# Kernel tuning notes

Measured on AMD Instinct MI355X. Metric: run time of the kernel, lower is better.

Reference implementation:

```python
import jax, jax.numpy as jnp
import numpy as np

B, N, D, H = 2, 2048, 1024, 16
HD = D // H
SCALE = HD ** -0.5


def setup_inputs() -> dict:
    key = jax.random.key(0)
    ks = jax.random.split(key, 5)
    s = D ** -0.5  # keep activations well-scaled like torch Linear init
    return {
        "x": jax.random.normal(ks[0], (B, N, D), jnp.float32),
        "Wq": jax.random.normal(ks[1], (D, D), jnp.float32) * s,
        "bq": jnp.zeros((D,), jnp.float32),
        "Wk": jax.random.normal(ks[2], (D, D), jnp.float32) * s,
        "bk": jnp.zeros((D,), jnp.float32),
        "Wv": jax.random.normal(ks[3], (D, D), jnp.float32) * s,
        "bv": jnp.zeros((D,), jnp.float32),
        "Wo": jax.random.normal(ks[4], (D, D), jnp.float32) * s,
        "bo": jnp.zeros((D,), jnp.float32),
    }


def reference(x, Wq, bq, Wk, bk, Wv, bv, Wo, bo):
    # projections: [B,N,D] -> [B,H,N,HD]
    def split_heads(t):
        return t.reshape(B, N, H, HD).transpose(0, 2, 1, 3)

    q = split_heads(x @ Wq + bq)
    k = split_heads(x @ Wk + bk)
    v = split_heads(x @ Wv + bv)
    # eager attention: explicit [B,H,N,N] scores, matching the torch module
    attn = jnp.einsum("bhnd,bhmd->bhnm", q, k) * SCALE
    attn = jax.nn.softmax(attn, axis=-1)
    out = jnp.einsum("bhnm,bhmd->bhnd", attn, v)
    out = out.transpose(0, 2, 1, 3).reshape(B, N, D)
    return out @ Wo + bo
```

## Files before the change

### kernel.cpp

```cpp
#include <hip/hip_runtime.h>
#include <hip/hip_bf16.h>

typedef __attribute__((ext_vector_type(8))) short bf16x8;
typedef __attribute__((ext_vector_type(4))) float f32x4;
typedef __attribute__((ext_vector_type(4))) unsigned short us4;
typedef __attribute__((ext_vector_type(8))) unsigned short us8;
typedef unsigned short u16;

#define NB 2
#define NSEQ 2048
#define DM 1024
#define NH 16
#define HD 64
#define NTOK (NB*NSEQ)
#define QK_SCALE (0.125f * 1.4426950408889634f)

__device__ __forceinline__ u16 f2b(float f) {
  __hip_bfloat16 h = __float2bfloat16(f);
  return __builtin_bit_cast(u16, h);
}

__device__ __forceinline__ unsigned cvtpk(float a, float b) {
  unsigned r;
  asm("v_cvt_pk_bf16_f32 %0, %1, %2" : "=v"(r) : "v"(a), "v"(b));
  return r;
}

__device__ __forceinline__ void gload16(const void* g, void* l) {
  __builtin_amdgcn_global_load_lds((__attribute__((address_space(1))) void*)g,
                                   (__attribute__((address_space(3))) void*)l, 16, 0, 0);
}

__global__ __launch_bounds__(256) void k_prep(const float* __restrict__ x, u16* __restrict__ xb,
                                              const float* __restrict__ W0, const float* __restrict__ W1,
                                              const float* __restrict__ W2, const float* __restrict__ W3,
                                              u16* __restrict__ T0, u16* __restrict__ T1,
                                              u16* __restrict__ T2, u16* __restrict__ T3) {
  __shared__ float tile[64][68];
  const int bid = blockIdx.x;
  if (bid >= 1024) {
    const int idx = ((bid - 1024) * 256 + threadIdx.x) * 8;
    const float4 v0 = *(const float4*)(x + idx);
    const float4 v1 = *(const float4*)(x + idx + 4);
    us8 o;
    o[0]=f2b(v0.x); o[1]=f2b(v0.y); o[2]=f2b(v0.z); o[3]=f2b(v0.w);
    o[4]=f2b(v1.x); o[5]=f2b(v1.y); o[6]=f2b(v1.z); o[7]=f2b(v1.w);
    *(us8*)(xb + idx) = o;
    return;
  }
  const int bz = bid >> 8, by = (bid >> 4) & 15, bx = bid & 15;
  const float* W = (bz == 0) ? W0 : (bz == 1) ? W1 : (bz == 2) ? W2 : W3;
  u16* WT = (bz == 0) ? T0 : (bz == 1) ? T1 : (bz == 2) ? T2 : T3;
  const int n0 = bx * 64, k0 = by * 64;
  const int tr = threadIdx.x >> 4, tc = (threadIdx.x & 15) * 4;
#pragma unroll
  for (int rr = 0; rr < 4; ++rr) {
    const int r = rr * 16 + tr;
    *(float4*)&tile[r][tc] = *(const float4*)&W[(size_t)(k0 + r) * DM + n0 + tc];
  }
  __syncthreads();
#pragma unroll
  for (int rr = 0; rr < 4; ++rr) {
    const int nr = rr * 16 + tr;
    us4 o;
#pragma unroll
    for (int e = 0; e < 4; ++e) o[e] = f2b(tile[tc + e][nr]);
    *(us4*)&WT[(size_t)(n0 + nr) * DM + k0 + tc] = o;
  }
}

__global__ __launch_bounds__(256) void k_gemm_qkv(
    const u16* __restrict__ xb,
    const u16* __restrict__ WqT, const u16* __restrict__ WkT, const u16* __restrict__ WvT,
    const float* __restrict__ bq, const float* __restrict__ bk, const float* __restrict__ bv,
    u16* __restrict__ Qb, u16* __restrict__ Kb, u16* __restrict__ Vtb)
{
  const int z = blockIdx.z;
  const bool isV = (z == 2);
  const u16* Ap = (z == 0) ? WqT : (z == 1) ? WkT : xb;
  const u16* Bt = isV ? WvT : xb;
  const float* bp = (z == 0) ? bq : (z == 1) ? bk : bv;
  const float scale = (z == 0) ? QK_SCALE : 1.0f;
  u16* outp = (z == 0) ? Qb : (z == 1) ? Kb : Vtb;
  const int i0 = isV ? blockIdx.x * 128 : blockIdx.y * 128;
  const int j0 = isV ? blockIdx.y * 128 : blockIdx.x * 128;

  __shared__ char smem[32 * 1024];
  const int tid = threadIdx.x, lane = tid & 63, wv = tid >> 6;
  const int li = lane & 15, g = lane >> 4;
  const int wi = wv >> 1, wj = wv & 1;

  f32x4 acc[4][4];
#pragma unroll
  for (int a = 0; a < 4; ++a)
#pragma unroll
    for (int b = 0; b < 4; ++b) acc[a][b] = f32x4{0.f, 0.f, 0.f, 0.f};

  auto stage = [&](int kt, int buf) {
#pragma unroll
    for (int c = 0; c < 2; ++c) {
      const int lg = c * 256 + tid;
      const int r = lg >> 2, ch = (lg & 3) ^ (r & 3);
      gload16(Ap + (size_t)(i0 + r) * 1024 + kt * 32 + ch * 8,
              smem + buf * 16384 + lg * 16);
      gload16(Bt + (size_t)(j0 + r) * 1024 + kt * 32 + ch * 8,
              smem + buf * 16384 + 8192 + lg * 16);
    }
  };

  stage(0, 0);

  for (int kt = 0; kt < 32; ++kt) {
    __syncthreads();
    if (kt + 1 < 32) stage(kt + 1, (kt + 1) & 1);
    const char* As = smem + (kt & 1) * 16384;
    const char* Bs = As + 8192;
    bf16x8 af[4], bfr[4];
#pragma unroll
    for (int it = 0; it < 4; ++it) {
      const int ri = 64 * wi + 16 * it + li;
      af[it] = *(const bf16x8*)(As + ri * 64 + ((g * 16) ^ ((ri & 3) << 4)));
      const int rj = 64 * wj + 16 * it + li;
      bfr[it] = *(const bf16x8*)(Bs + rj * 64 + ((g * 16) ^ ((rj & 3) << 4)));
    }
#pragma unroll
    for (int it = 0; it < 4; ++it)
#pragma unroll
      for (int jt = 0; jt < 4; ++jt)
        acc[it][jt] = __builtin_amdgcn_mfma_f32_16x16x32_bf16(af[it], bfr[jt], acc[it][jt], 0, 0, 0);
  }

#pragma unroll
  for (int it = 0; it < 4; ++it) {
    const int ib = i0 + 64 * wi + 16 * it + 4 * g;
    f32x4 b4;
    if (!isV) b4 = *(const f32x4*)(bp + ib);
#pragma unroll
    for (int jt = 0; jt < 4; ++jt) {
      const int j = j0 + 64 * wj + 16 * jt + li;
      f32x4 v = acc[it][jt];
      if (!isV) {
        v += b4;
        v *= scale;
        us4 pk; pk[0]=f2b(v[0]); pk[1]=f2b(v[1]); pk[2]=f2b(v[2]); pk[3]=f2b(v[3]);
        *(us4*)(outp + (size_t)j * 1024 + ib) = pk;
      } else {
        const float bj = bp[j];
        v[0] += bj; v[1] += bj; v[2] += bj; v[3] += bj;
        us4 pk; pk[0]=f2b(v[0]); pk[1]=f2b(v[1]); pk[2]=f2b(v[2]); pk[3]=f2b(v[3]);
        const size_t addr = ((size_t)(ib >> 11) * 1024 + j) * 2048 + (ib & 2047);
        *(us4*)(outp + addr) = pk;
      }
    }
  }
}

__global__ __launch_bounds__(256) void k_gemm_out(
    const u16* __restrict__ A, const u16* __restrict__ Bt, const float* __restrict__ bias,
    float* __restrict__ outp)
{
  __shared__ char smem[48 * 1024];
  const int tid = threadIdx.x, lane = tid & 63, wv = tid >> 6;
  const int li = lane & 15, g = lane >> 4;
  const int i0 = blockIdx.y * 128, j0 = blockIdx.x * 64;

  f32x4 acc[2][4];
#pragma unroll
  for (int a = 0; a < 2; ++a)
#pragma unroll
    for (int b = 0; b < 4; ++b) acc[a][b] = f32x4{0.f, 0.f, 0.f, 0.f};

  auto stage = [&](int kt, int buf) {
#pragma unroll
    for (int c = 0; c < 4; ++c) {
      const int lg = c * 256 + tid;
      const int r = lg >> 3, ch = (lg & 7) ^ (r & 7);
      gload16(A + (size_t)(i0 + r) * 1024 + kt * 64 + ch * 8,
              smem + buf * 24576 + lg * 16);
    }
#pragma unroll
    for (int c = 0; c < 2; ++c) {
      const int lg = c * 256 + tid;
      const int r = lg >> 3, ch = (lg & 7) ^ (r & 7);
      gload16(Bt + (size_t)(j0 + r) * 1024 + kt * 64 + ch * 8,
              smem + buf * 24576 + 16384 + lg * 16);
    }
  };

  stage(0, 0);

  for (int kt = 0; kt < 16; ++kt) {
    __syncthreads();
    if (kt + 1 < 16) stage(kt + 1, (kt + 1) & 1);
    const char* As = smem + (kt & 1) * 24576;
    const char* Bs = As + 16384;
#pragma unroll
    for (int ks = 0; ks < 2; ++ks) {
      bf16x8 af[2], bfr[4];
#pragma unroll
      for (int it = 0; it < 2; ++it) {
        const int ri = 32 * wv + 16 * it + li;
        af[it] = *(const bf16x8*)(As + ri * 128 + ((ks * 64 + g * 16) ^ ((ri & 7) << 4)));
      }
#pragma unroll
      for (int jt = 0; jt < 4; ++jt) {
        const int rj = 16 * jt + li;
        bfr[jt] = *(const bf16x8*)(Bs + rj * 128 + ((ks * 64 + g * 16) ^ ((rj & 7) << 4)));
      }
#pragma unroll
      for (int it = 0; it < 2; ++it)
#pragma unroll
        for (int jt = 0; jt < 4; ++jt)
          acc[it][jt] = __builtin_amdgcn_mfma_f32_16x16x32_bf16(af[it], bfr[jt], acc[it][jt], 0, 0, 0);
    }
  }

#pragma unroll
  for (int it = 0; it < 2; ++it) {
    const int ib = i0 + 32 * wv + 16 * it + 4 * g;
    const f32x4 b4 = *(const f32x4*)(bias + ib);
#pragma unroll
    for (int jt = 0; jt < 4; ++jt) {
      const int j = j0 + 16 * jt + li;
      f32x4 v = acc[it][jt] + b4;
      *(f32x4*)(outp + (size_t)j * 1024 + ib) = v;
    }
  }
}

__global__ __launch_bounds__(256, 2) void k_attn(const u16* __restrict__ Q, const u16* __restrict__ K,
                                                 const u16* __restrict__ Vt, u16* __restrict__ O)
{
  __shared__ char smem[64 * 1024];
  const int tid = threadIdx.x, lane = tid & 63, w = tid >> 6;
  const int li = lane & 15, g = lane >> 4;

  const int vid = blockIdx.x;
  const int u = vid >> 3;
  const int bh = (vid & 7) * 4 + (u >> 4);
  const int qt = u & 15;
  const int b = bh >> 4, h = bh & 15;
  const int n0 = qt * 128;
  const size_t tokbase = (size_t)b * NSEQ;
  const int iq = 16 * w + li;

  bf16x8 qf[2][2];
#pragma unroll
  for (int grp = 0; grp < 2; ++grp)
#pragma unroll
    for (int ks = 0; ks < 2; ++ks)
      qf[grp][ks] = *(const bf16x8*)(Q + (tokbase + n0 + 64 * grp + iq) * 1024 + h * 64 + 32 * ks + 8 * g);

  bf16x8 ones;
#pragma unroll
  for (int e = 0; e < 8; ++e) ones[e] = (short)0x3F80;

  f32x4 oacc[2][4];
#pragma unroll
  for (int grp = 0; grp < 2; ++grp)
#pragma unroll
    for (int dt = 0; dt < 4; ++dt) oacc[grp][dt] = f32x4{0.f, 0.f, 0.f, 0.f};
  f32x4 ls[2] = {f32x4{0.f,0.f,0.f,0.f}, f32x4{0.f,0.f,0.f,0.f}};

  const u16* Kb = K + tokbase * 1024 + h * 64;
  const u16* Vb = Vt + (size_t)bh * 64 * 2048;

  auto stage = [&](int t, int buf) {
    const int jn = t * 64;
#pragma unroll
    for (int c = 0; c < 2; ++c) {
      const int lg = c * 256 + tid;
      const int r = lg >> 3, ch = (lg & 7) ^ (r & 7);
      gload16(Kb + (size_t)(jn + r) * 1024 + ch * 8, smem + buf * 8192 + (c * 256 + w * 64) * 16);
      gload16(Vb + (size_t)r * 2048 + jn + ch * 8, smem + 24576 + buf * 8192 + (c * 256 + w * 64) * 16);
    }
  };

  auto sync2 = [&]() {
    asm volatile("s_waitcnt vmcnt(4)" ::: "memory");
    __builtin_amdgcn_sched_barrier(0);
    __builtin_amdgcn_s_barrier();
    __builtin_amdgcn_sched_barrier(0);
  };

  auto body = [&](int buf) {
    const char* Ks = smem + buf * 8192;
    const char* Vs = smem + 24576 + buf * 8192;

    f32x4 s[2][4];
#pragma unroll
    for (int grp = 0; grp < 2; ++grp)
#pragma unroll
      for (int jt = 0; jt < 4; ++jt) s[grp][jt] = f32x4{0.f, 0.f, 0.f, 0.f};
    __builtin_amdgcn_s_setprio(1);
#pragma unroll
    for (int ks = 0; ks < 2; ++ks) {
#pragma unroll
      for (int jt = 0; jt < 4; ++jt) {
        const int rj = 16 * jt + li;
        bf16x8 a = *(const bf16x8*)(Ks + rj * 128 + ((ks * 64 + g * 16) ^ ((rj & 7) << 4)));
        s[0][jt] = __builtin_amdgcn_mfma_f32_16x16x32_bf16(a, qf[0][ks], s[0][jt], 0, 0, 0);
        s[1][jt] = __builtin_amdgcn_mfma_f32_16x16x32_bf16(a, qf[1][ks], s[1][jt], 0, 0, 0);
      }
    }
    __builtin_amdgcn_s_setprio(0);

#pragma unroll
    for (int grp = 0; grp < 2; ++grp) {
      const int row = iq + 64 * grp;
      char* Pr = smem + 49152 + row * 128;
      const int swz = (row & 7) << 4;
#pragma unroll
      for (int jt = 0; jt < 4; ++jt) {
        uint2 pk;
        pk.x = cvtpk(exp2f(s[grp][jt][0]), exp2f(s[grp][jt][1]));
        pk.y = cvtpk(exp2f(s[grp][jt][2]), exp2f(s[grp][jt][3]));
        *(uint2*)(Pr + ((32 * jt + 8 * g) ^ swz)) = pk;
      }
    }

    __builtin_amdgcn_s_setprio(1);
#pragma unroll
    for (int ks = 0; ks < 2; ++ks) {
      const int kb = ks * 64 + g * 16;
      bf16x8 bpv0 = *(const bf16x8*)(smem + 49152 + iq * 128 + (kb ^ ((iq & 7) << 4)));
      bf16x8 bpv1 = *(const bf16x8*)(smem + 49152 + (iq + 64) * 128 + (kb ^ ((iq & 7) << 4)));
      ls[0] = __builtin_amdgcn_mfma_f32_16x16x32_bf16(ones, bpv0, ls[0], 0, 0, 0);
      ls[1] = __builtin_amdgcn_mfma_f32_16x16x32_bf16(ones, bpv1, ls[1], 0, 0, 0);
#pragma unroll
      for (int dt = 0; dt < 4; ++dt) {
        const int rd = 16 * dt + li;
        bf16x8 av = *(const bf16x8*)(Vs + rd * 128 + (kb ^ ((rd & 7) << 4)));
        oacc[0][dt] = __builtin_amdgcn_mfma_f32_16x16x32_bf16(av, bpv0, oacc[0][dt], 0, 0, 0);
        oacc[1][dt] = __builtin_amdgcn_mfma_f32_16x16x32_bf16(av, bpv1, oacc[1][dt], 0, 0, 0);
      }
    }
    __builtin_amdgcn_s_setprio(0);
  };

  stage(0, 0);
  stage(1, 1);

#pragma unroll 1
  for (int tt = 0; tt < 10; ++tt) {
#pragma unroll
    for (int uu = 0; uu < 3; ++uu) {
      const int t = tt * 3 + uu;
      sync2();
      stage(t + 2, (uu + 2) % 3);
      body(uu);
    }
  }
  sync2();
  body(0);
  asm volatile("s_waitcnt vmcnt(0)" ::: "memory");
  __builtin_amdgcn_sched_barrier(0);
  __builtin_amdgcn_s_barrier();
  __builtin_amdgcn_sched_barrier(0);
  body(1);

#pragma unroll
  for (int grp = 0; grp < 2; ++grp) {
    const float inv = 1.f / ls[grp][0];
    const size_t obase = (tokbase + n0 + 64 * grp + iq) * 1024 + h * 64;
#pragma unroll
    for (int dt = 0; dt < 4; ++dt) {
      us4 pk;
#pragma unroll
      for (int e = 0; e < 4; ++e) pk[e] = f2b(oacc[grp][dt][e] * inv);
      *(us4*)(O + obase + 16 * dt + 4 * g) = pk;
    }
  }
}

extern "C" void kernel_launch(void* const* d_in, const int* in_sizes, int n_in,
                              void* d_out, int out_size, void* d_ws, size_t ws_size,
                              hipStream_t stream) {
  const float* x  = (const float*)d_in[0];
  const float* Wq = (const float*)d_in[1];
  const float* bq = (const float*)d_in[2];
  const float* Wk = (const float*)d_in[3];
  const float* bk = (const float*)d_in[4];
  const float* Wv = (const float*)d_in[5];
  const float* bv = (const float*)d_in[6];
  const float* Wo = (const float*)d_in[7];
  const float* bo = (const float*)d_in[8];

  char* ws = (char*)d_ws;
  u16* xb  = (u16*)(ws);
  u16* WqT = (u16*)(ws + (8  << 20));
  u16* WkT = (u16*)(ws + (10 << 20));
  u16* WvT = (u16*)(ws + (12 << 20));
  u16* WoT = (u16*)(ws + (14 << 20));
  u16* Qb  = (u16*)(ws + (16 << 20));
  u16* Kb  = (u16*)(ws + (24 << 20));
  u16* Vtb = (u16*)(ws + (32 << 20));
  u16* Ob  = (u16*)(ws + (40 << 20));

  k_prep<<<3072, 256, 0, stream>>>(x, xb, Wq, Wk, Wv, Wo, WqT, WkT, WvT, WoT);

  k_gemm_qkv<<<dim3(32, 8, 3), 256, 0, stream>>>(xb, WqT, WkT, WvT, bq, bk, bv, Qb, Kb, Vtb);

  k_attn<<<512, 256, 0, stream>>>(Qb, Kb, Vtb, Ob);

  k_gemm_out<<<dim3(64, 8), 256, 0, stream>>>(WoT, Ob, bo, (float*)d_out);
}
```

Before: 118.9 us.

## Switch attention to 32x32x16 MFMA and keep P in registers via permlane swap

The attention kernel moves from 16x16x32 to 32x32x16 bf16 MFMA tiles, with each wave owning 32 query rows. The exponentiated scores are repacked in registers with v_permlane32_swap into the B-operand layout for the PV product, so the shared-memory round trip for P is gone and LDS shrinks from 64KB to 48KB. This is meant to cut LDS traffic and barriers-free stores/loads per tile and raise MFMA efficiency. The cost is more accumulator registers (f32x16 accumulators) and a dependence on the lane layout for the permlane swap being correct.

Measured after the change: 120.4 us. No clear change (+1.3%).

```diff
diff --git a/kernel.cpp b/kernel.cpp
--- a/kernel.cpp
+++ b/kernel.cpp
@@ -3,6 +3,8 @@
 
 typedef __attribute__((ext_vector_type(8))) short bf16x8;
 typedef __attribute__((ext_vector_type(4))) float f32x4;
+typedef __attribute__((ext_vector_type(16))) float f32x16;
+typedef __attribute__((ext_vector_type(4))) unsigned int u32x4;
 typedef __attribute__((ext_vector_type(4))) unsigned short us4;
 typedef __attribute__((ext_vector_type(8))) unsigned short us8;
 typedef unsigned short u16;
@@ -231,38 +233,32 @@
 __global__ __launch_bounds__(256, 2) void k_attn(const u16* __restrict__ Q, const u16* __restrict__ K,
                                                  const u16* __restrict__ Vt, u16* __restrict__ O)
 {
-  __shared__ char smem[64 * 1024];
+  __shared__ char smem[48 * 1024];
   const int tid = threadIdx.x, lane = tid & 63, w = tid >> 6;
-  const int li = lane & 15, g = lane >> 4;
+  const int rl = lane & 31, h2 = lane >> 5;
 
   const int vid = blockIdx.x;
   const int u = vid >> 3;
   const int bh = (vid & 7) * 4 + (u >> 4);
   const int qt = u & 15;
-  const int b = bh >> 4, h = bh & 15;
+  const int b = bh >> 4, hh = bh & 15;
   const int n0 = qt * 128;
   const size_t tokbase = (size_t)b * NSEQ;
-  const int iq = 16 * w + li;
-
-  bf16x8 qf[2][2];
-#pragma unroll
-  for (int grp = 0; grp < 2; ++grp)
-#pragma unroll
-    for (int ks = 0; ks < 2; ++ks)
-      qf[grp][ks] = *(const bf16x8*)(Q + (tokbase + n0 + 64 * grp + iq) * 1024 + h * 64 + 32 * ks + 8 * g);
+
+  bf16x8 qf[4];
+#pragma unroll
+  for (int sp = 0; sp < 4; ++sp)
+    qf[sp] = *(const bf16x8*)(Q + (tokbase + n0 + 32 * w + rl) * 1024 + hh * 64 + sp * 16 + 8 * h2);
 
   bf16x8 ones;
 #pragma unroll
   for (int e = 0; e < 8; ++e) ones[e] = (short)0x3F80;
 
-  f32x4 oacc[2][4];
-#pragma unroll
-  for (int grp = 0; grp < 2; ++grp)
-#pragma unroll
-    for (int dt = 0; dt < 4; ++dt) oacc[grp][dt] = f32x4{0.f, 0.f, 0.f, 0.f};
-  f32x4 ls[2] = {f32x4{0.f,0.f,0.f,0.f}, f32x4{0.f,0.f,0.f,0.f}};
-
-  const u16* Kb = K + tokbase * 1024 + h * 64;
+  f32x16 oacc[2], ls;
+#pragma unroll
+  for (int i = 0; i < 16; ++i) { oacc[0][i] = 0.f; oacc[1][i] = 0.f; ls[i] = 0.f; }
+
+  const u16* Kb = K + tokbase * 1024 + hh * 64;
   const u16* Vb = Vt + (size_t)bh * 64 * 2048;
 
   auto stage = [&](int t, int buf) {
@@ -286,53 +282,50 @@
   auto body = [&](int buf) {
     const char* Ks = smem + buf * 8192;
     const char* Vs = smem + 24576 + buf * 8192;
-
-    f32x4 s[2][4];
-#pragma unroll
-    for (int grp = 0; grp < 2; ++grp)
-#pragma unroll
-      for (int jt = 0; jt < 4; ++jt) s[grp][jt] = f32x4{0.f, 0.f, 0.f, 0.f};
+    const int swz = (rl & 7) << 4;
+
+    f32x16 s0, s1;
+#pragma unroll
+    for (int i = 0; i < 16; ++i) { s0[i] = 0.f; s1[i] = 0.f; }
     __builtin_amdgcn_s_setprio(1);
 #pragma unroll
-    for (int ks = 0; ks < 2; ++ks) {
-#pragma unroll
-      for (int jt = 0; jt < 4; ++jt) {
-        const int rj = 16 * jt + li;
-        bf16x8 a = *(const bf16x8*)(Ks + rj * 128 + ((ks * 64 + g * 16) ^ ((rj & 7) << 4)));
-        s[0][jt] = __builtin_amdgcn_mfma_f32_16x16x32_bf16(a, qf[0][ks], s[0][jt], 0, 0, 0);
-        s[1][jt] = __builtin_amdgcn_mfma_f32_16x16x32_bf16(a, qf[1][ks], s[1][jt], 0, 0, 0);
-      }
+    for (int sp = 0; sp < 4; ++sp) {
+      const int off = 32 * sp + 16 * h2;
+      bf16x8 k0 = *(const bf16x8*)(Ks + rl * 128 + (off ^ swz));
+      s0 = __builtin_amdgcn_mfma_f32_32x32x16_bf16(k0, qf[sp], s0, 0, 0, 0);
+      bf16x8 k1 = *(const bf16x8*)(Ks + (32 + rl) * 128 + (off ^ swz));
+      s1 = __builtin_amdgcn_mfma_f32_32x32x16_bf16(k1, qf[sp], s1, 0, 0, 0);
     }
     __builtin_amdgcn_s_setprio(0);
 
-#pragma unroll
-    for (int grp = 0; grp < 2; ++grp) {
-      const int row = iq + 64 * grp;
-      char* Pr = smem + 49152 + row * 128;
-      const int swz = (row & 7) << 4;
-#pragma unroll
-      for (int jt = 0; jt < 4; ++jt) {
-        uint2 pk;
-        pk.x = cvtpk(exp2f(s[grp][jt][0]), exp2f(s[grp][jt][1]));
-        pk.y = cvtpk(exp2f(s[grp][jt][2]), exp2f(s[grp][jt][3]));
-        *(uint2*)(Pr + ((32 * jt + 8 * g) ^ swz)) = pk;
-      }
+    bf16x8 pf[4];
+#pragma unroll
+    for (int s = 0; s < 4; ++s) {
+      const int bb = 8 * (s & 1);
+      float e0, e1, e2, e3, e4, e5, e6, e7;
+      if (s < 2) {
+        e0 = exp2f(s0[bb+0]); e1 = exp2f(s0[bb+1]); e2 = exp2f(s0[bb+2]); e3 = exp2f(s0[bb+3]);
+        e4 = exp2f(s0[bb+4]); e5 = exp2f(s0[bb+5]); e6 = exp2f(s0[bb+6]); e7 = exp2f(s0[bb+7]);
+      } else {
+        e0 = exp2f(s1[bb+0]); e1 = exp2f(s1[bb+1]); e2 = exp2f(s1[bb+2]); e3 = exp2f(s1[bb+3]);
+        e4 = exp2f(s1[bb+4]); e5 = exp2f(s1[bb+5]); e6 = exp2f(s1[bb+6]); e7 = exp2f(s1[bb+7]);
+      }
+      unsigned a0 = cvtpk(e0, e1), b0 = cvtpk(e4, e5);
+      asm("v_permlane32_swap_b32 %0, %1" : "+v"(a0), "+v"(b0));
+      unsigned a1 = cvtpk(e2, e3), b1 = cvtpk(e6, e7);
+      asm("v_permlane32_swap_b32 %0, %1" : "+v"(a1), "+v"(b1));
+      u32x4 wd; wd[0] = a0; wd[1] = a1; wd[2] = b0; wd[3] = b1;
+      pf[s] = __builtin_bit_cast(bf16x8, wd);
     }
 
     __builtin_amdgcn_s_setprio(1);
 #pragma unroll
-    for (int ks = 0; ks < 2; ++ks) {
-      const int kb = ks * 64 + g * 16;
-      bf16x8 bpv0 = *(const bf16x8*)(smem + 49152 + iq * 128 + (kb ^ ((iq & 7) << 4)));
-      bf16x8 bpv1 = *(const bf16x8*)(smem + 49152 + (iq + 64) * 128 + (kb ^ ((iq & 7) << 4)));
-      ls[0] = __builtin_amdgcn_mfma_f32_16x16x32_bf16(ones, bpv0, ls[0], 0, 0, 0);
-      ls[1] = __builtin_amdgcn_mfma_f32_16x16x32_bf16(ones, bpv1, ls[1], 0, 0, 0);
-#pragma unroll
-      for (int dt = 0; dt < 4; ++dt) {
-        const int rd = 16 * dt + li;
-        bf16x8 av = *(const bf16x8*)(Vs + rd * 128 + (kb ^ ((rd & 7) << 4)));
-        oacc[0][dt] = __builtin_amdgcn_mfma_f32_16x16x32_bf16(av, bpv0, oacc[0][dt], 0, 0, 0);
-        oacc[1][dt] = __builtin_amdgcn_mfma_f32_16x16x32_bf16(av, bpv1, oacc[1][dt], 0, 0, 0);
+    for (int s = 0; s < 4; ++s) {
+      ls = __builtin_amdgcn_mfma_f32_32x32x16_bf16(ones, pf[s], ls, 0, 0, 0);
+#pragma unroll
+      for (int d = 0; d < 2; ++d) {
+        bf16x8 av = *(const bf16x8*)(Vs + (32 * d + rl) * 128 + ((32 * s + 16 * h2) ^ swz));
+        oacc[d] = __builtin_amdgcn_mfma_f32_32x32x16_bf16(av, pf[s], oacc[d], 0, 0, 0);
       }
     }
     __builtin_amdgcn_s_setprio(0);
@@ -359,18 +352,17 @@
   __builtin_amdgcn_sched_barrier(0);
   body(1);
 
-#pragma unroll
-  for (int grp = 0; grp < 2; ++grp) {
-    const float inv = 1.f / ls[grp][0];
-    const size_t obase = (tokbase + n0 + 64 * grp + iq) * 1024 + h * 64;
-#pragma unroll
-    for (int dt = 0; dt < 4; ++dt) {
+  const float inv = 1.f / ls[0];
+  const size_t obase = (tokbase + n0 + 32 * w + rl) * 1024 + hh * 64;
+#pragma unroll
+  for (int d = 0; d < 2; ++d)
+#pragma unroll
+    for (int v = 0; v < 4; ++v) {
       us4 pk;
 #pragma unroll
-      for (int e = 0; e < 4; ++e) pk[e] = f2b(oacc[grp][dt][e] * inv);
-      *(us4*)(O + obase + 16 * dt + 4 * g) = pk;
-    }
-  }
+      for (int e = 0; e < 4; ++e) pk[e] = f2b(oacc[d][4 * v + e] * inv);
+      *(us4*)(O + obase + 32 * d + 8 * v + 4 * h2) = pk;
+    }
 }
 
 extern "C" void kernel_launch(void* const* d_in, const int* in_sizes, int n_in,
```
